# Optimization experiments

Hardware: AMD Instinct MI355X
Metric: run time of the kernel (lower is better)

The kernel has to match this reference:

```python
import jax, jax.numpy as jnp
import numpy as np

B, N_SRC, N_TGT = 8, 1024, 1024
IN_CH, OUT_CH, HEADS = 256, 256, 4
HEAD_DIM = OUT_CH // HEADS
NEG_INF = jnp.float32(-1000000000.0)
EPS = 1e-12


def setup_inputs() -> dict:
    key = jax.random.key(0)
    ks = jax.random.split(key, 8)
    x_source = jax.random.normal(ks[0], (B, N_SRC, IN_CH), dtype=jnp.float32)
    x_target = jax.random.normal(ks[1], (B, N_TGT, IN_CH), dtype=jnp.float32)
    adj_vals = jax.random.uniform(ks[2], (B, N_TGT, N_SRC), dtype=jnp.float32)
    keep = jax.random.uniform(ks[3], (B, N_TGT, N_SRC)) < 0.3
    adj = jnp.where(keep, adj_vals, 0.0)
    mask = jnp.ones((B, N_TGT), dtype=bool)
    # parameters (xavier-ish scale)
    sw = float(np.sqrt(6.0 / (IN_CH + HEADS * HEAD_DIM)))
    W_src = jax.random.uniform(ks[4], (HEADS * HEAD_DIM, IN_CH), minval=-sw, maxval=sw, dtype=jnp.float32)
    W_tgt = jax.random.uniform(ks[5], (HEADS * HEAD_DIM, IN_CH), minval=-sw, maxval=sw, dtype=jnp.float32)
    sa = float(np.sqrt(6.0 / (HEADS + HEAD_DIM)))
    att_src = jax.random.uniform(ks[6], (HEADS, HEAD_DIM), minval=-sa, maxval=sa, dtype=jnp.float32)
    att_tgt = jax.random.uniform(ks[7], (HEADS, HEAD_DIM), minval=-sa, maxval=sa, dtype=jnp.float32)
    bias = jnp.zeros((OUT_CH,), dtype=jnp.float32)
    return {"x_source": x_source, "x_target": x_target, "adj": adj, "mask": mask,
            "W_src": W_src, "W_tgt": W_tgt, "att_src": att_src, "att_tgt": att_tgt, "bias": bias}


def reference(x_source, x_target, adj, mask, W_src, W_tgt, att_src, att_tgt, bias):
    b, n_src, _ = x_source.shape
    n_tgt = x_target.shape[1]
    h, d = att_src.shape
    h_src = (x_source @ W_src.T).reshape(b, n_src, h, d)   # (B,Ns,H,D)
    h_tgt = (x_target @ W_tgt.T).reshape(b, n_tgt, h, d)   # (B,Nt,H,D)
    a_src = jnp.einsum('bshd,hd->bsh', h_src, att_src)
    a_tgt = jnp.einsum('bthd,hd->bth', h_tgt, att_tgt)
    scores = a_tgt[:, :, None, :] + a_src[:, None, :, :]   # (B,Nt,Ns,H)
    scores = jnp.where(scores >= 0, scores, 0.2 * scores)  # leaky_relu(0.2)
    edge_mask = (adj != 0) & mask[:, :, None] & mask[:, None, :]  # (B,Nt,Ns)
    em = edge_mask[..., None]                               # (B,Nt,Ns,1)
    scores = jnp.where(em, scores, NEG_INF)
    attn = jax.nn.softmax(scores, axis=2)
    attn = attn * em.astype(attn.dtype)
    attn = attn / (attn.sum(axis=2, keepdims=True) + EPS)
    out = jnp.einsum('btsh,bshd->bthd', attn, h_src).reshape(b, n_tgt, h * d)
    out = out + bias
    out = out * mask[:, :, None].astype(out.dtype)
    return out
```

## Files before the change

kernel.cpp:

```cpp
#include <hip/hip_runtime.h>


typedef __attribute__((ext_vector_type(4))) float f32x4;
typedef __attribute__((ext_vector_type(2))) float f32x2;
typedef __attribute__((ext_vector_type(8))) short bf16x8;
typedef __attribute__((ext_vector_type(4))) short s16x4;
typedef __attribute__((ext_vector_type(4))) unsigned u32x4;

#define MFMA_BF16 __builtin_amdgcn_mfma_f32_16x16x32_bf16

static __device__ __forceinline__ short f2bf(float f) {
    unsigned u = __builtin_bit_cast(unsigned, f);
    u = (u + 0x7FFFu + ((u >> 16) & 1u)) >> 16;
    return (short)u;
}

#if __has_builtin(__builtin_amdgcn_cvt_pk_bf16_f32)
typedef __attribute__((ext_vector_type(2))) __bf16 bf2_t;
static __device__ __forceinline__ unsigned pkbf(float a, float b) {
    bf2_t p = __builtin_amdgcn_cvt_pk_bf16_f32(a, b);
    return __builtin_bit_cast(unsigned, p);
}
#else
static __device__ __forceinline__ unsigned pkbf(float a, float b) {
    return (unsigned)(unsigned short)f2bf(a) | ((unsigned)(unsigned short)f2bf(b) << 16);
}
#endif

static __device__ __forceinline__ bf16x8 cvt8(f32x4 a0, f32x4 a1) {
    u32x4 w;
    w[0] = pkbf(a0[0], a0[1]);
    w[1] = pkbf(a0[2], a0[3]);
    w[2] = pkbf(a1[0], a1[1]);
    w[3] = pkbf(a1[2], a1[3]);
    return __builtin_bit_cast(bf16x8, w);
}

static __device__ __forceinline__ void dma16(const void* g, void* l) {
    __builtin_amdgcn_global_load_lds(
        (const __attribute__((address_space(1))) unsigned*)g,
        (__attribute__((address_space(3))) unsigned*)l, 16, 0, 0);
}

__global__ __launch_bounds__(256) void k_miscw(
    const float* __restrict__ Ws, const float* __restrict__ Wt,
    unsigned short* __restrict__ Wf)
{
    __shared__ __align__(16) float wt[16][260];
    const int cb   = blockIdx.x;
    const int tid  = threadIdx.x;
    const int side = cb >> 4;
    const int grp  = cb & 15;
    const int cg   = grp >> 2, nt = grp & 3;
    const float* src = side ? Wt : Ws;
    const int row = tid >> 4, k0 = (tid & 15) * 16;
    const float* p = src + (size_t)(grp * 16 + row) * 256 + k0;
#pragma unroll
    for (int j = 0; j < 4; ++j)
        *(f32x4*)&wt[row][k0 + j * 4] = *(const f32x4*)(p + j * 4);
    __syncthreads();
#pragma unroll
    for (int i = 0; i < 2; ++i) {
        int e = i * 256 + tid;
        int sc = e >> 6, dl = e & 63, q = dl >> 4, n15 = dl & 15;
        f32x4 a0 = *(const f32x4*)&wt[n15][sc * 32 + q * 8];
        f32x4 a1 = *(const f32x4*)&wt[n15][sc * 32 + q * 8 + 4];
        size_t off = ((((size_t)(side * 4 + cg) * 8 + sc) * 4 + nt) * 64 + dl) * 8;
        *(bf16x8*)(Wf + off) = cvt8(a0, a1);
    }
}

__global__ __launch_bounds__(512) void k_proj(
    const float* __restrict__ xs, const float* __restrict__ xt,
    const unsigned short* __restrict__ Wf,
    const float* __restrict__ att_s, const float* __restrict__ att_t,
    unsigned short* __restrict__ hTf,
    float* __restrict__ aS2,
    float* __restrict__ aT)
{
    __shared__ __align__(16) unsigned short sh[256 * 72];
    const int blk   = blockIdx.x;
    const bool isSrc = blk < 128;
    const int blkL  = isSrc ? blk : blk - 128;
    const float* __restrict__ x = isSrc ? xs : xt;
    const int side = isSrc ? 0 : 1;
    const float* __restrict__ att = isSrc ? att_s : att_t;

    const int row0 = blkL * 64;
    const int b    = row0 >> 10;
    const int t0   = row0 & 1023;
    const int tid  = threadIdx.x;
    const int wave = tid >> 6, lane = tid & 63;
    const int quad = lane >> 4, l15 = lane & 15;
    const int rh   = wave >> 2;
    const int cg   = wave & 3;

    unsigned short (*xt_)[264] = (unsigned short(*)[264])sh;

    {
        const int row = tid >> 3, kq = (tid & 7) * 32;
        const float* p = x + (size_t)(row0 + row) * 256 + kq;
#pragma unroll
        for (int j = 0; j < 4; ++j) {
            f32x4 a0 = *(const f32x4*)(p + j * 8);
            f32x4 a1 = *(const f32x4*)(p + j * 8 + 4);
            *(bf16x8*)&xt_[row][kq + j * 8] = cvt8(a0, a1);
        }
    }
    __syncthreads();

    f32x4 acc[2][4];
#pragma unroll
    for (int i = 0; i < 2; i++)
#pragma unroll
        for (int j = 0; j < 4; j++) acc[i][j] = (f32x4)0.f;

    const unsigned short* wbase = Wf + (size_t)(side * 4 + cg) * 16384;
    auto loadWf = [&](int sc, bf16x8* wf) {
#pragma unroll
        for (int nt = 0; nt < 4; ++nt)
            wf[nt] = *(const bf16x8*)(wbase + ((size_t)(sc * 4 + nt) * 64 + lane) * 8);
    };
    auto mmaStep = [&](int sc, const bf16x8* wf) {
        bf16x8 af[2];
#pragma unroll
        for (int mt = 0; mt < 2; ++mt)
            af[mt] = *(const bf16x8*)&xt_[rh * 32 + mt * 16 + l15][sc * 32 + quad * 8];
#pragma unroll
        for (int mt = 0; mt < 2; ++mt)
#pragma unroll
            for (int nt = 0; nt < 4; ++nt)
                acc[mt][nt] = MFMA_BF16(af[mt], wf[nt], acc[mt][nt], 0, 0, 0);
    };

    bf16x8 WA[4], WB[4];
    loadWf(0, WA);
#pragma unroll 1
    for (int sc = 0; sc < 8; sc += 2) {
        loadWf(sc + 1, WB);
        mmaStep(sc, WA);
        loadWf(sc + 2 < 8 ? sc + 2 : 0, WA);
        mmaStep(sc + 1, WB);
    }

    float attv[4];
#pragma unroll
    for (int nt = 0; nt < 4; nt++) attv[nt] = att[cg * 64 + nt * 16 + l15];
#pragma unroll
    for (int mt = 0; mt < 2; mt++)
#pragma unroll
        for (int r = 0; r < 4; r++) {
            float v = acc[mt][0][r] * attv[0] + acc[mt][1][r] * attv[1]
                    + acc[mt][2][r] * attv[2] + acc[mt][3][r] * attv[3];
            v += __shfl_xor(v, 1);
            v += __shfl_xor(v, 2);
            v += __shfl_xor(v, 4);
            v += __shfl_xor(v, 8);
            if (l15 == 0) {
                int idx = t0 + rh * 32 + mt * 16 + quad * 4 + r;
                if (isSrc) {
                    f32x2 pq;
                    pq[0] = __expf(v);
                    pq[1] = __expf(0.2f * v);
                    *(f32x2*)(aS2 + ((((size_t)(b * 4 + cg)) << 10) + idx) * 2) = pq;
                } else {
                    aT[((b * 4 + cg) << 10) + idx] = v;
                }
            }
        }

    if (isSrc) {
        __syncthreads();
        unsigned short* tile = sh;
#pragma unroll
        for (int mt = 0; mt < 2; mt++)
#pragma unroll
            for (int nt = 0; nt < 4; nt++)
#pragma unroll
                for (int r = 0; r < 4; r++) {
                    int sl = rh * 32 + mt * 16 + quad * 4 + r;
                    int c  = cg * 64 + nt * 16 + l15;
                    tile[c * 72 + sl] = (unsigned short)f2bf(acc[mt][nt][r]);
                }
        __syncthreads();
        const int sc0 = t0 >> 5;
#pragma unroll
        for (int i = 0; i < 4; ++i) {
            int e   = i * 512 + tid;
            int hh  = e >> 9, scl = (e >> 8) & 1, nt = (e >> 6) & 3, dl = e & 63;
            int q   = dl >> 4, n15 = dl & 15;
            bf16x8 v = *(const bf16x8*)&tile[(hh * 64 + nt * 16 + n15) * 72
                                             + scl * 32 + q * 8];
            size_t off = ((((size_t)(b * 4 + hh) * 32 + sc0 + scl) * 4 + nt) * 64 + dl) * 8;
            *(bf16x8*)(hTf + off) = v;
        }
    }
}

__global__ __launch_bounds__(512, 2) void k_attn(
    const float* __restrict__ adj,
    const unsigned short* __restrict__ hTf,
    const float* __restrict__ aS2,
    const float* __restrict__ aT,
    const float* __restrict__ bias,
    float* __restrict__ out)
{
    __shared__ __align__(16) float aSL[4][1024][2];
    __shared__ unsigned long long mLT[32][17];
    __shared__ float mrg[4][64][41];

    const int blk = blockIdx.x;
    const int b   = blk & 7;
    const int t0  = (blk >> 3) << 5;
    const int tid = threadIdx.x;
    const int wave = tid >> 6, lane = tid & 63;
    const int quad = lane >> 4, l15 = lane & 15;
    const int h = wave >> 1, kk = wave & 1;

#pragma unroll
    for (int j = 0; j < 4; ++j) {
        int g0 = j * 512 + wave * 64;
        dma16(aS2 + ((size_t)b << 13) + (size_t)(g0 + lane) * 4,
              (char*)aSL + (size_t)g0 * 16);
    }
#pragma unroll 1
    for (int pp = 0; pp < 8; pp += 4) {
        float v[4];
#pragma unroll
        for (int u = 0; u < 4; ++u) {
            int p = wave * 64 + (pp + u) * 8 + 0;
            (void)p;
            int pi = wave * 64 + (pp + u) * 8;
            (void)pi;
            int pr = wave * 64 + (pp + u) * 8;
            (void)pr;
            v[u] = 0.f;
        }
        break;
    }
    {
#pragma unroll 1
        for (int p0 = 0; p0 < 64; p0 += 8) {
            float v[8];
#pragma unroll
            for (int u = 0; u < 8; ++u) {
                int p = wave * 64 + p0 + u;
                int t = p >> 4, wd = p & 15;
                v[u] = adj[((size_t)((b << 10) + t0 + t) << 10) + wd * 64 + lane];
            }
#pragma unroll
            for (int u = 0; u < 8; ++u) {
                int p = wave * 64 + p0 + u;
                int t = p >> 4, wd = p & 15;
                unsigned long long bm = __ballot(v[u] != 0.f);
                if (lane == 0) mLT[t][wd] = bm;
            }
        }
    }

    float Pt[2], Qt[2];
#pragma unroll
    for (int f = 0; f < 2; ++f) {
        float a_t = aT[((b * 4 + h) << 10) + t0 + f * 16 + l15];
        Pt[f] = __expf(a_t);
        Qt[f] = __expf(0.2f * a_t);
    }

    const unsigned short* __restrict__ vb = hTf + (size_t)(b * 4 + h) * 65536;

    const short onev = (l15 == 0) ? (short)0x3F80 : (short)0;
    const bf16x8 onesB = {onev, onev, onev, onev, onev, onev, onev, onev};

    f32x4 acc[2][4];
#pragma unroll
    for (int f = 0; f < 2; ++f)
#pragma unroll
        for (int nt = 0; nt < 4; nt++) acc[f][nt] = (f32x4)0.f;
    f32x4 accS[2] = {(f32x4)0.f, (f32x4)0.f};

    struct Frag { bf16x8 bf[8]; };

    auto issue = [&](int c, Frag& F) {
#pragma unroll
        for (int ks = 0; ks < 2; ++ks)
#pragma unroll
            for (int nt = 0; nt < 4; ++nt) {
                int sc = kk * 16 + 2 * c + ks;
                F.bf[nt * 2 + ks] = *(const bf16x8*)(
                    vb + ((size_t)(sc * 4 + nt) * 64 + lane) * 8);
            }
    };
    auto compute = [&](int c, const Frag& F) {
        unsigned long long mv0 = mLT[l15][kk * 8 + c];
        unsigned long long mv1 = mLT[16 + l15][kk * 8 + c];
#pragma unroll
        for (int ks = 0; ks < 2; ++ks) {
            const float* ap = &aSL[h][kk * 512 + c * 64 + ks * 32 + quad * 8][0];
            f32x4 pk[4];
#pragma unroll
            for (int q = 0; q < 4; ++q) pk[q] = *(const f32x4*)(ap + q * 4);
#pragma unroll
            for (int f = 0; f < 2; ++f) {
                unsigned mb = (unsigned)((f ? mv1 : mv0)
                                         >> (ks * 32 + quad * 8)) & 0xFFu;
                float e[8];
#pragma unroll
                for (int j = 0; j < 8; j++) {
                    float Ps = pk[j >> 1][(j & 1) * 2];
                    float Qs = pk[j >> 1][(j & 1) * 2 + 1];
                    float ev = fmaxf(Pt[f] * Ps, Qt[f] * Qs);
                    e[j] = (mb & (1u << j)) ? ev : 0.f;
                }
                u32x4 w;
                w[0] = pkbf(e[0], e[1]); w[1] = pkbf(e[2], e[3]);
                w[2] = pkbf(e[4], e[5]); w[3] = pkbf(e[6], e[7]);
                bf16x8 pa = __builtin_bit_cast(bf16x8, w);
#pragma unroll
                for (int nt = 0; nt < 4; ++nt)
                    acc[f][nt] = MFMA_BF16(pa, F.bf[nt * 2 + ks], acc[f][nt], 0, 0, 0);
                accS[f] = MFMA_BF16(pa, onesB, accS[f], 0, 0, 0);
            }
        }
    };

    Frag A, Bf;
    issue(0, A);
    __syncthreads();
#pragma unroll 1
    for (int c = 0; c < 8; c += 2) {
        issue(c + 1, Bf);
        compute(c, A);
        issue(c + 2 < 8 ? c + 2 : 0, A);
        compute(c + 1, Bf);
    }

    if (kk) {
#pragma unroll
        for (int f = 0; f < 2; ++f)
#pragma unroll
            for (int nt = 0; nt < 4; ++nt)
                *(f32x4*)&mrg[h][lane][f * 16 + nt * 4] = acc[f][nt];
        *(f32x4*)&mrg[h][lane][32] = accS[0];
        *(f32x4*)&mrg[h][lane][36] = accS[1];
    }
    __syncthreads();
    if (!kk) {
#pragma unroll
        for (int f = 0; f < 2; ++f)
#pragma unroll
            for (int nt = 0; nt < 4; ++nt)
                acc[f][nt] += *(const f32x4*)&mrg[h][lane][f * 16 + nt * 4];
        accS[0] += *(const f32x4*)&mrg[h][lane][32];
        accS[1] += *(const f32x4*)&mrg[h][lane][36];
#pragma unroll
        for (int f = 0; f < 2; ++f)
#pragma unroll
            for (int nt = 0; nt < 4; ++nt) {
                float bi = bias[h * 64 + nt * 16 + l15];
#pragma unroll
                for (int r = 0; r < 4; r++) {
                    float rs = __shfl(accS[f][r], quad << 4);
                    int trow = t0 + f * 16 + quad * 4 + r;
                    out[(size_t)((b << 10) + trow) * 256 + h * 64 + nt * 16 + l15]
                        = acc[f][nt][r] / (rs + 1e-12f) + bi;
                }
            }
    }
}

extern "C" void kernel_launch(void* const* d_in, const int* in_sizes, int n_in,
                              void* d_out, int out_size, void* d_ws, size_t ws_size,
                              hipStream_t stream) {
    const float* xs   = (const float*)d_in[0];
    const float* xt   = (const float*)d_in[1];
    const float* adj  = (const float*)d_in[2];
    const float* Ws   = (const float*)d_in[4];
    const float* Wt   = (const float*)d_in[5];
    const float* atts = (const float*)d_in[6];
    const float* attt = (const float*)d_in[7];
    const float* bias = (const float*)d_in[8];
    float* out = (float*)d_out;

    unsigned short* hTf = (unsigned short*)d_ws;
    float* aS2 = (float*)((char*)d_ws + (size_t)4 * 1024 * 1024);
    float* aT  = aS2 + 8 * 4 * 1024 * 2;
    unsigned short* Wf = (unsigned short*)(aT + 8 * 4 * 1024);

    hipLaunchKernelGGL(k_miscw, dim3(32), dim3(256), 0, stream, Ws, Wt, Wf);
    hipLaunchKernelGGL(k_proj, dim3(256), dim3(512), 0, stream,
                       xs, xt, Wf, atts, attt, hTf, aS2, aT);
    hipLaunchKernelGGL(k_attn, dim3(256), dim3(512), 0, stream,
                       adj, hTf, aS2, aT, bias, out);
}
```

Baseline: 121.6 us.

## Move adjacency bitmask construction from attention kernel into projection kernel

Result: slower. 125.0 us (+2.8%).

```diff
diff --git a/kernel.cpp b/kernel.cpp
--- a/kernel.cpp
+++ b/kernel.cpp
@@ -74,6 +74,8 @@
     const float* __restrict__ xs, const float* __restrict__ xt,
     const unsigned short* __restrict__ Wf,
     const float* __restrict__ att_s, const float* __restrict__ att_t,
+    const float* __restrict__ adj,
+    unsigned long long* __restrict__ m64,
     unsigned short* __restrict__ hTf,
     float* __restrict__ aS2,
     float* __restrict__ aT)
@@ -195,10 +197,26 @@
             *(bf16x8*)(hTf + off) = v;
         }
     }
+
+    {
+        const int wbase2 = blk * 512 + wave * 64;
+#pragma unroll 1
+        for (int p0 = 0; p0 < 64; p0 += 8) {
+            float v[8];
+#pragma unroll
+            for (int u = 0; u < 8; ++u)
+                v[u] = adj[((size_t)(wbase2 + p0 + u) << 6) + lane];
+#pragma unroll
+            for (int u = 0; u < 8; ++u) {
+                unsigned long long bm = __ballot(v[u] != 0.f);
+                if (lane == 0) m64[wbase2 + p0 + u] = bm;
+            }
+        }
+    }
 }
 
 __global__ __launch_bounds__(512, 2) void k_attn(
-    const float* __restrict__ adj,
+    const unsigned long long* __restrict__ m64,
     const unsigned short* __restrict__ hTf,
     const float* __restrict__ aS2,
     const float* __restrict__ aT,
@@ -223,39 +241,9 @@
         dma16(aS2 + ((size_t)b << 13) + (size_t)(g0 + lane) * 4,
               (char*)aSL + (size_t)g0 * 16);
     }
-#pragma unroll 1
-    for (int pp = 0; pp < 8; pp += 4) {
-        float v[4];
-#pragma unroll
-        for (int u = 0; u < 4; ++u) {
-            int p = wave * 64 + (pp + u) * 8 + 0;
-            (void)p;
-            int pi = wave * 64 + (pp + u) * 8;
-            (void)pi;
-            int pr = wave * 64 + (pp + u) * 8;
-            (void)pr;
-            v[u] = 0.f;
-        }
-        break;
-    }
     {
-#pragma unroll 1
-        for (int p0 = 0; p0 < 64; p0 += 8) {
-            float v[8];
-#pragma unroll
-            for (int u = 0; u < 8; ++u) {
-                int p = wave * 64 + p0 + u;
-                int t = p >> 4, wd = p & 15;
-                v[u] = adj[((size_t)((b << 10) + t0 + t) << 10) + wd * 64 + lane];
-            }
-#pragma unroll
-            for (int u = 0; u < 8; ++u) {
-                int p = wave * 64 + p0 + u;
-                int t = p >> 4, wd = p & 15;
-                unsigned long long bm = __ballot(v[u] != 0.f);
-                if (lane == 0) mLT[t][wd] = bm;
-            }
-        }
+        int row = tid >> 4, wd = tid & 15;
+        mLT[row][wd] = m64[((size_t)((b << 10) + t0 + row) << 4) + wd];
     }
 
     float Pt[2], Qt[2];
@@ -385,10 +373,11 @@
     float* aS2 = (float*)((char*)d_ws + (size_t)4 * 1024 * 1024);
     float* aT  = aS2 + 8 * 4 * 1024 * 2;
     unsigned short* Wf = (unsigned short*)(aT + 8 * 4 * 1024);
+    unsigned long long* m64 = (unsigned long long*)(Wf + 2 * 256 * 256);
 
     hipLaunchKernelGGL(k_miscw, dim3(32), dim3(256), 0, stream, Ws, Wt, Wf);
     hipLaunchKernelGGL(k_proj, dim3(256), dim3(512), 0, stream,
-                       xs, xt, Wf, atts, attt, hTf, aS2, aT);
+                       xs, xt, Wf, atts, attt, adj, m64, hTf, aS2, aT);
     hipLaunchKernelGGL(k_attn, dim3(256), dim3(512), 0, stream,
-                       adj, hTf, aS2, aT, bias, out);
-}
+                       m64, hTf, aS2, aT, bias, out);
+}
```
